# Performance work log

Measured on AMD Instinct MI355X. Metric: run time of the kernel, lower is better.

Reference implementation:

```python
import jax, jax.numpy as jnp
from jax import lax
import numpy as np

STRIDE = 1
PADDING = 1
DILATION = 1


def setup_inputs() -> dict:
    key = jax.random.key(0)
    k1, k2, k3, k4 = jax.random.split(key, 4)
    B, Cin, Cout, H, W, K, G = 32, 256, 256, 56, 56, 3, 8
    x = jax.random.normal(k1, (B, Cin, H, W), dtype=jnp.float32)
    conv = jax.random.normal(k2, (Cout, Cin, K, K), dtype=jnp.float32)
    S = jax.random.normal(k3, (Cin, G), dtype=jnp.float32)
    T = jax.random.normal(k4, (Cout, G), dtype=jnp.float32)
    return {"x": x, "conv": conv, "S": S, "T": T}


def reference(x, conv, S, T):
    # Faithful to FLGC.forward (training path).
    Cin = S.shape[0]
    Cout = T.shape[0]
    s_hat = jax.nn.softmax(S, axis=1)            # [Cin, G]
    t_hat = jax.nn.softmax(T, axis=1)            # [Cout, G]
    s = jnp.argmax(s_hat, axis=1)                # group id per input channel
    t = jnp.argmax(t_hat, axis=1)                # group id per output filter
    # Input channel c is scaled by s_hat[c, s[c]] inside its group.
    x_sc = x * s_hat[jnp.arange(Cin), s][None, :, None, None]
    # Filter o uses weight conv[o,c] * t_hat[o, t[o]] only where s[c] == t[o];
    # masking weights to zero elsewhere makes one dense conv equal the per-group convs.
    gate = (s[None, :] == t[:, None]).astype(conv.dtype)          # [Cout, Cin]
    w = conv * t_hat[jnp.arange(Cout), t][:, None, None, None] * gate[:, :, None, None]
    out_full = lax.conv_general_dilated(
        x_sc, w,
        window_strides=(STRIDE, STRIDE),
        padding=[(PADDING, PADDING), (PADDING, PADDING)],
        rhs_dilation=(DILATION, DILATION),
    )  # [B, Cout, H', W'], channel o = group-conv output of filter o
    # Original concatenates group outputs (channels ordered by perm = stable sort of t),
    # then indexes that with perm again: final[:, j] = out_full[:, perm[perm[j]]].
    perm = jnp.argsort(t * Cout + jnp.arange(Cout))  # stable group-major order
    return out_full[:, perm[perm]]
```

## Files before the change

kernel.cpp:

```cpp
#include <hip/hip_runtime.h>

#define M_SI    0
#define M_SO    256
#define M_CLIST 512
#define M_FLIST 768
#define M_DEST  1024
#define M_CBASE 1280
#define M_FBASE 1288
#define M_CCNT  1296
#define M_FCNT  1304
#define M_WOFFE 1312
#define WPACK_BYTE_OFF 16384
#define XR_BYTE_OFF   (4u << 20)
#define SLOT_ELEMS    3444736ull
#define SLOT_BYTES    (SLOT_ELEMS * 2ull)

typedef short bf16x8 __attribute__((ext_vector_type(8)));
typedef float f32x4  __attribute__((ext_vector_type(4)));

__device__ __forceinline__ unsigned short f2bf(float f) {
    unsigned u = __float_as_uint(f);
    u += 0x7fffu + ((u >> 16) & 1u);
    return (unsigned short)(u >> 16);
}

__device__ __forceinline__ void gl_lds16(const void* g, void* l) {
    __builtin_amdgcn_global_load_lds((const __attribute__((address_space(1))) unsigned int*)g,
                                     (__attribute__((address_space(3))) unsigned int*)l, 16, 0, 0);
}

__global__ __launch_bounds__(256) void flgc_setup(const float* __restrict__ S,
                                                  const float* __restrict__ T,
                                                  int* __restrict__ meta) {
    __shared__ float si[256], so[256];
    __shared__ int gin[256], gout[256];
    __shared__ int cnt_in[8], cnt_out[8], cb[8], fb[8];
    __shared__ int perm[256], destl[256];
    const int c = threadIdx.x;

    {
        float m = S[c * 8]; int am = 0;
        for (int k = 1; k < 8; ++k) { float v = S[c * 8 + k]; if (v > m) { m = v; am = k; } }
        float s = 0.f;
        for (int k = 0; k < 8; ++k) s += expf(S[c * 8 + k] - m);
        si[c] = 1.0f / s; gin[c] = am;
    }
    {
        float m = T[c * 8]; int am = 0;
        for (int k = 1; k < 8; ++k) { float v = T[c * 8 + k]; if (v > m) { m = v; am = k; } }
        float s = 0.f;
        for (int k = 0; k < 8; ++k) s += expf(T[c * 8 + k] - m);
        so[c] = 1.0f / s; gout[c] = am;
    }
    __syncthreads();
    const int g = gin[c], go = gout[c];
    int r1 = 0, r2 = 0;
    for (int i = 0; i < c; ++i) { r1 += (gin[i] == g); r2 += (gout[i] == go); }
    if (c < 8) {
        int n1 = 0, n2 = 0;
        for (int i = 0; i < 256; ++i) { n1 += (gin[i] == c); n2 += (gout[i] == c); }
        cnt_in[c] = n1; cnt_out[c] = n2;
    }
    __syncthreads();
    if (c == 0) {
        int a = 0, b = 0;
        for (int k = 0; k < 8; ++k) { cb[k] = a; a += cnt_in[k]; fb[k] = b; b += cnt_out[k]; }
    }
    __syncthreads();
    meta[M_CLIST + cb[g] + r1] = c;
    perm[fb[go] + r2] = c;
    __syncthreads();
    const int ppc = perm[perm[c]];
    destl[ppc] = c;
    __syncthreads();
    ((float*)meta)[M_SI + c] = si[c];
    ((float*)meta)[M_SO + c] = so[c];
    meta[M_FLIST + c] = perm[c];
    meta[M_DEST + c]  = destl[c];
    if (c < 8) {
        meta[M_CBASE + c] = cb[c];
        meta[M_FBASE + c] = fb[c];
        meta[M_CCNT + c]  = cnt_in[c];
        meta[M_FCNT + c]  = cnt_out[c];
    }
    if (c == 0) {
        int a = 0;
        for (int k = 0; k < 8; ++k) {
            meta[M_WOFFE + k] = a;
            const int nq  = (cnt_in[k] + 31) >> 5;
            const int mfa = (cnt_out[k] + 15) >> 4;
            a += nq * mfa * 9 * 512;
        }
        meta[M_WOFFE + 8] = a;
    }
}

__global__ void flgc_pack(const float* __restrict__ conv, const int* __restrict__ meta,
                          unsigned short* __restrict__ wpack) {
    const float* si = (const float*)meta + M_SI;
    const float* so = (const float*)meta + M_SO;
    const int total = meta[M_WOFFE + 8];
    for (int idx = blockIdx.x * blockDim.x + threadIdx.x; idx < total;
         idx += gridDim.x * blockDim.x) {
        int gg = 0;
        while (gg < 7 && idx >= meta[M_WOFFE + gg + 1]) ++gg;
        const int local = idx - meta[M_WOFFE + gg];
        const int fcnt = meta[M_FCNT + gg], ccnt = meta[M_CCNT + gg];
        const int mfall = (fcnt + 15) >> 4;
        const int fragidx = local >> 9, e = local & 511;
        const int lane = e >> 3, j = e & 7;
        const int tap = fragidx % 9, t2 = fragidx / 9;
        const int mf = t2 % mfall, q = t2 / mfall;
        const int fl = mf * 16 + (lane & 15);
        const int cl = q * 32 + (lane >> 4) * 8 + j;
        float v = 0.f;
        if (fl < fcnt && cl < ccnt) {
            const int F  = meta[M_FLIST + meta[M_FBASE + gg] + fl];
            const int CH = meta[M_CLIST + meta[M_CBASE + gg] + cl];
            v = conv[(F * 256 + CH) * 9 + tap] * si[CH] * so[F];
        }
        wpack[idx] = f2bf(v);
    }
}

__global__ __launch_bounds__(256) void flgc_reorder(const float* __restrict__ x,
                                                    const int* __restrict__ meta,
                                                    unsigned short* __restrict__ xr) {
    __shared__ float lds[32][65];
    const int r = blockIdx.x;
    const int b = blockIdx.y;
    const int slot = blockIdx.z;
    const int g = slot >> 1, q = slot & 1;
    const int ccnt = meta[M_CCNT + g];
    int nq = (ccnt + 31) >> 5; if (nq > 2) nq = 2;
    if (q >= nq) return;
    const int cbas = meta[M_CBASE + g];
    const int row = r - 1;
    const int colx = threadIdx.x & 63;
    const int cl0 = threadIdx.x >> 6;
    const int ic = colx - 1;
    const bool ok = ((unsigned)row < 56u) && ((unsigned)ic < 56u);

    int chn[8];
#pragma unroll
    for (int i = 0; i < 8; ++i) {
        const int cgl = q * 32 + cl0 + i * 4;
        chn[i] = (cgl < ccnt) ? meta[M_CLIST + cbas + cgl] : -1;
    }
    const float* xb = x + (size_t)b * 256 * 3136 + row * 56 + ic;
    float v[8];
#pragma unroll
    for (int i = 0; i < 8; ++i) v[i] = 0.f;
#pragma unroll
    for (int i = 0; i < 8; ++i)
        if (ok && chn[i] >= 0) v[i] = xb[(size_t)chn[i] * 3136];
#pragma unroll
    for (int i = 0; i < 8; ++i) lds[cl0 + i * 4][colx] = v[i];
    __syncthreads();

    unsigned short* dst = xr + (size_t)(slot * 32 + b) * 107648ull + r * 58 * 32;
    for (int i = threadIdx.x; i < 58 * 8; i += 256) {
        const int col = i >> 3, c8 = i & 7;
        const int chunk = c8 >> 1, lo = (c8 & 1) * 4;
        const int cl4 = chunk * 8 + lo;
        ushort4 pk = make_ushort4(f2bf(lds[cl4 + 0][col]), f2bf(lds[cl4 + 1][col]),
                                  f2bf(lds[cl4 + 2][col]), f2bf(lds[cl4 + 3][col]));
        const int schunk = chunk ^ ((col >> 1) & 3);
        *(ushort4*)&dst[col * 32 + schunk * 8 + lo] = pk;
    }
}


#define TAPS(Q)                                                                              \
    _Pragma("unroll") for (int tap = 0; tap < 9; ++tap) {                                    \
        const int dr = tap / 3, dc = tap - dr * 3;                                           \
        const int rowb = ((wv + dr) * 58) << 6;                                              \
        _Pragma("unroll") for (int cg = 0; cg < 4; ++cg) {                                   \
            const bf16x8 Bv = *(const bf16x8*)((const char*)xb + rowb + addrc[cg][dc]);      \
            _Pragma("unroll") for (int mf = 0; mf < MFE; ++mf)                               \
                acc[mf][cg] = __builtin_amdgcn_mfma_f32_16x16x32_bf16(                       \
                    A[Q][mf][tap], Bv, acc[mf][cg], 0, 0, 0);                                \
        }                                                                                    \
    }

template <int NQ, int MFE>
__device__ __forceinline__ void conv_pass(
    const unsigned short* __restrict__ wpack, const unsigned short* __restrict__ xr,
    float* __restrict__ out, unsigned short* xbufA, unsigned short* xbufB,
    const int (&ocv)[2][4], int b, int g, int z, int mf0, int mfall, int woffe,
    int lane, int wv) {
    const int nn = lane & 15, kg = lane >> 4;
    bf16x8 A[NQ][MFE][9];
#pragma unroll
    for (int q = 0; q < NQ; ++q)
#pragma unroll
        for (int mf = 0; mf < MFE; ++mf)
#pragma unroll
            for (int tap = 0; tap < 9; ++tap)
                A[q][mf][tap] = *(const bf16x8*)
                    &wpack[woffe + ((size_t)((q * mfall) + (mf0 + mf)) * 9 + tap) * 512 + lane * 8];
    int addrc[4][3];
#pragma unroll
    for (int cg = 0; cg < 4; ++cg)
#pragma unroll
        for (int dc = 0; dc < 3; ++dc) {
            int ccol = cg * 16 + nn + dc; if (ccol > 57) ccol = 57;
            addrc[cg][dc] = (ccol << 6) + ((kg ^ ((ccol >> 1) & 3)) << 4);
        }
    const int ns = (z < 2) ? 4 : 3;
    const int P = ns * NQ;
    const int base = wv * 348;
    {
        const char* src = (const char*)(xr + (size_t)((g * 2) * 32 + b) * 107648ull
                                        + (size_t)(4 * z) * 1856);
        char* dstb = (char*)xbufA;
#pragma unroll
        for (int j = 0; j < 5; ++j)
            gl_lds16(src + (size_t)(base + j * 64 + lane) * 16, dstb + (base + j * 64) * 16);
        if (lane < 28)
            gl_lds16(src + (size_t)(base + 320 + lane) * 16, dstb + (base + 320) * 16);
    }
    f32x4 acc[MFE][4];
    for (int p = 0; p < P; ++p) {
        if (p + 1 < P) {
            const int pn = p + 1;
            const int sp = z + 4 * (pn / NQ);
            const int qp = (NQ == 2) ? (pn & 1) : 0;
            const char* src = (const char*)(xr + (size_t)((g * 2 + qp) * 32 + b) * 107648ull
                                            + (size_t)(4 * sp) * 1856);
            char* dstb = (char*)((pn & 1) ? xbufB : xbufA);
#pragma unroll
            for (int j = 0; j < 5; ++j)
                gl_lds16(src + (size_t)(base + j * 64 + lane) * 16, dstb + (base + j * 64) * 16);
            if (lane < 28)
                gl_lds16(src + (size_t)(base + 320 + lane) * 16, dstb + (base + 320) * 16);
            asm volatile("s_waitcnt vmcnt(6)" ::: "memory");
        } else {
            asm volatile("s_waitcnt vmcnt(0)" ::: "memory");
        }
        __builtin_amdgcn_s_barrier();
        __builtin_amdgcn_sched_barrier(0);
        const unsigned short* xb = (p & 1) ? xbufB : xbufA;
        const int s = z + 4 * ((NQ == 2) ? (p >> 1) : p);
        if (NQ == 1 || (p & 1) == 0) {
#pragma unroll
            for (int mf = 0; mf < MFE; ++mf)
#pragma unroll
                for (int cg = 0; cg < 4; ++cg) acc[mf][cg] = (f32x4){0.f, 0.f, 0.f, 0.f};
        }
        if (NQ == 2 && (p & 1)) { TAPS(1) } else { TAPS(0) }
        if (NQ == 1 || (p & 1)) {
            const int h = 4 * s + wv;
#pragma unroll
            for (int mf = 0; mf < MFE; ++mf)
#pragma unroll
                for (int reg = 0; reg < 4; ++reg) {
                    const int oc = ocv[mf][reg];
                    if (oc >= 0) {
                        float* op = out + ((size_t)(b * 256 + oc) * 56 + h) * 56;
#pragma unroll
                        for (int cg = 0; cg < 4; ++cg) {
                            const int col = cg * 16 + nn;
                            if (col < 56) op[col] = acc[mf][cg][reg];
                        }
                    }
                }
        }
        __builtin_amdgcn_sched_barrier(0);
        __builtin_amdgcn_s_barrier();
    }
}

__global__ __launch_bounds__(256, 2) void flgc_conv_r(const int* __restrict__ meta,
                                                      const unsigned short* __restrict__ wpack,
                                                      const unsigned short* __restrict__ xr,
                                                      float* __restrict__ out) {
    __shared__ __align__(16) unsigned short xbufA[11136];
    __shared__ __align__(16) unsigned short xbufB[11136];
    const int b = blockIdx.x, g = blockIdx.y, z = blockIdx.z;
    const int tid = threadIdx.x, lane = tid & 63, wv = tid >> 6;
    const int ccnt = meta[M_CCNT + g], fcnt = meta[M_FCNT + g];
    const int fbas = meta[M_FBASE + g], woffe = meta[M_WOFFE + g];
    int nq = (ccnt + 31) >> 5; if (nq > 2) nq = 2;
    const int mfall = (fcnt + 15) >> 4;
    if (mfall == 0) return;
    const int nn = lane & 15;

    for (int mf0 = 0; mf0 < mfall; mf0 += 2) {
        const int mfe = min(2, mfall - mf0);
        int ocv[2][4];
#pragma unroll
        for (int mf = 0; mf < 2; ++mf)
#pragma unroll
            for (int reg = 0; reg < 4; ++reg) {
                const int fl = (mf0 + mf) * 16 + (lane >> 4) * 4 + reg;
                ocv[mf][reg] = (mf < mfe && fl < fcnt)
                    ? meta[M_DEST + meta[M_FLIST + fbas + fl]] : -1;
            }
        if (nq == 0) {
            const int ns = (z < 2) ? 4 : 3;
            for (int si = 0; si < ns; ++si) {
                const int h = 4 * (z + 4 * si) + wv;
#pragma unroll
                for (int mf = 0; mf < 2; ++mf)
#pragma unroll
                    for (int reg = 0; reg < 4; ++reg)
                        if (ocv[mf][reg] >= 0) {
                            float* op = out + ((size_t)(b * 256 + ocv[mf][reg]) * 56 + h) * 56;
#pragma unroll
                            for (int cg = 0; cg < 4; ++cg) {
                                const int col = cg * 16 + nn;
                                if (col < 56) op[col] = 0.f;
                            }
                        }
            }
            continue;
        }
        if (nq == 1) {
            if (mfe == 2) conv_pass<1, 2>(wpack, xr, out, xbufA, xbufB, ocv, b, g, z, mf0, mfall, woffe, lane, wv);
            else          conv_pass<1, 1>(wpack, xr, out, xbufA, xbufB, ocv, b, g, z, mf0, mfall, woffe, lane, wv);
        } else {
            if (mfe == 2) conv_pass<2, 2>(wpack, xr, out, xbufA, xbufB, ocv, b, g, z, mf0, mfall, woffe, lane, wv);
            else          conv_pass<2, 1>(wpack, xr, out, xbufA, xbufB, ocv, b, g, z, mf0, mfall, woffe, lane, wv);
        }
    }
}

__global__ __launch_bounds__(256, 2) void flgc_conv_mfma(const float* __restrict__ x,
                                                         const int* __restrict__ meta,
                                                         const unsigned short* __restrict__ wpack,
                                                         float* __restrict__ out) {
    __shared__ __align__(16) unsigned short xlds[10 * 4 * 64 * 8];
    __shared__ __align__(16) unsigned short wlds[4 * 9 * 512];
    const int g = blockIdx.z, b = blockIdx.y, h0 = blockIdx.x * 8;
    const int tid = threadIdx.x, lane = tid & 63, wv = tid >> 6;
    const int ccnt = meta[M_CCNT + g], fcnt = meta[M_FCNT + g];
    const int cbas = meta[M_CBASE + g], fbas = meta[M_FBASE + g];
    const int woffe = meta[M_WOFFE + g];
    const int nq = (ccnt + 31) >> 5, mfall = (fcnt + 15) >> 4;
    if (mfall == 0) return;
    const int n = lane & 15, kgl = lane >> 4;
    const int prow = 2 * wv + (n >> 3);
    const int pcol = n & 7;

    for (int mf0 = 0; mf0 < mfall; mf0 += 4) {
        const int mfe = min(4, mfall - mf0);
        f32x4 acc[4][7];
#pragma unroll
        for (int mf = 0; mf < 4; ++mf)
#pragma unroll
            for (int cg = 0; cg < 7; ++cg) acc[mf][cg] = (f32x4){0.f, 0.f, 0.f, 0.f};

        for (int q = 0; q < nq; ++q) {
            __syncthreads();
            for (int widx = wv; widx < mfe * 9; widx += 4) {
                const int mf = widx / 9, tap = widx - mf * 9;
                const unsigned short* src =
                    wpack + woffe + (((q * mfall) + mf0 + mf) * 9 + tap) * 512 + lane * 8;
                *(bf16x8*)&wlds[(mf * 9 + tap) * 512 + lane * 8] = *(const bf16x8*)src;
            }
            for (int i = tid; i < 80 * 64; i += 256) {
                const int colx = i & 63, t = i >> 6;
                const int rr = t >> 3, cq = t & 7;
                const int c0 = q * 32 + cq * 4;
                const int row = h0 + rr - 1, ic = colx - 1;
                float v0 = 0.f, v1 = 0.f, v2 = 0.f, v3 = 0.f;
                if ((unsigned)row < 56u && (unsigned)ic < 56u) {
                    const float* xp = x + (size_t)(b * 256) * 3136 + row * 56 + ic;
                    if (c0 + 0 < ccnt) v0 = xp[(size_t)meta[M_CLIST + cbas + c0 + 0] * 3136];
                    if (c0 + 1 < ccnt) v1 = xp[(size_t)meta[M_CLIST + cbas + c0 + 1] * 3136];
                    if (c0 + 2 < ccnt) v2 = xp[(size_t)meta[M_CLIST + cbas + c0 + 2] * 3136];
                    if (c0 + 3 < ccnt) v3 = xp[(size_t)meta[M_CLIST + cbas + c0 + 3] * 3136];
                }
                ushort4 pk = make_ushort4(f2bf(v0), f2bf(v1), f2bf(v2), f2bf(v3));
                *(ushort4*)&xlds[(((rr * 4 + (cq >> 1)) * 64 + colx) << 3) + ((cq & 1) << 2)] = pk;
            }
            __syncthreads();
#pragma unroll
            for (int tap = 0; tap < 9; ++tap) {
                const int dr = tap / 3, dcp = tap - dr * 3;
                bf16x8 A[4];
#pragma unroll
                for (int mf = 0; mf < 4; ++mf)
                    if (mf < mfe)
                        A[mf] = *(bf16x8*)&wlds[(mf * 9 + tap) * 512 + lane * 8];
                const int row_r = prow + dr;
                const int xbase = ((row_r * 4 + kgl) * 64) << 3;
#pragma unroll
                for (int cg = 0; cg < 7; ++cg) {
                    const int cc = cg * 8 + pcol + dcp;
                    const bf16x8 B = *(bf16x8*)&xlds[xbase + (cc << 3)];
#pragma unroll
                    for (int mf = 0; mf < 4; ++mf)
                        if (mf < mfe)
                            acc[mf][cg] = __builtin_amdgcn_mfma_f32_16x16x32_bf16(
                                A[mf], B, acc[mf][cg], 0, 0, 0);
                }
            }
        }
#pragma unroll
        for (int mf = 0; mf < 4; ++mf) {
            if (mf < mfe) {
#pragma unroll
                for (int reg = 0; reg < 4; ++reg) {
                    const int fl = (mf0 + mf) * 16 + (lane >> 4) * 4 + reg;
                    if (fl < fcnt) {
                        const int F  = meta[M_FLIST + fbas + fl];
                        const int oc = meta[M_DEST + F];
                        float* op = out + ((size_t)(b * 256 + oc) * 56 + (h0 + prow)) * 56 + pcol;
#pragma unroll
                        for (int cg = 0; cg < 7; ++cg)
                            op[cg * 8] = acc[mf][cg][reg];
                    }
                }
            }
        }
    }
}

extern "C" void kernel_launch(void* const* d_in, const int* in_sizes, int n_in,
                              void* d_out, int out_size, void* d_ws, size_t ws_size,
                              hipStream_t stream) {
    const float* x    = (const float*)d_in[0];
    const float* conv = (const float*)d_in[1];
    const float* S    = (const float*)d_in[2];
    const float* T    = (const float*)d_in[3];
    float* out = (float*)d_out;
    int* meta = (int*)d_ws;
    unsigned short* wpack = (unsigned short*)((char*)d_ws + WPACK_BYTE_OFF);
    unsigned short* xr    = (unsigned short*)((char*)d_ws + XR_BYTE_OFF);

    flgc_setup<<<1, 256, 0, stream>>>(S, T, meta);
    flgc_pack<<<256, 256, 0, stream>>>(conv, meta, wpack);

    const size_t need = (size_t)XR_BYTE_OFF + 16ull * SLOT_BYTES + 65536;
    if (ws_size >= need) {
        flgc_reorder<<<dim3(58, 32, 16), 256, 0, stream>>>(x, meta, xr);
        flgc_conv_r<<<dim3(32, 8, 4), 256, 0, stream>>>(meta, wpack, xr, out);
    } else {
        flgc_conv_mfma<<<dim3(7, 32, 8), 256, 0, stream>>>(x, meta, wpack, out);
    }
}
```

Baseline: 127.2 us.

## Reload weight fragments per pass and widen filter tile to three MFMA blocks

Weight fragments are now loaded from global memory on every pipeline step instead of being held in registers for the whole pass. The register space this frees lets each block process up to three 16-filter MFMA tiles at once instead of two, so the input row tile staged in LDS is reused across more filters and fewer passes over the input are needed. The channel-chunk count becomes a runtime value instead of a template parameter. The cost is repeated global or cache loads of the weights on each step, plus possible register pressure from the larger accumulator array.

```diff
diff --git a/kernel.cpp b/kernel.cpp
--- a/kernel.cpp
+++ b/kernel.cpp
@@ -170,35 +170,13 @@
     }
 }
 
-
-#define TAPS(Q)                                                                              \
-    _Pragma("unroll") for (int tap = 0; tap < 9; ++tap) {                                    \
-        const int dr = tap / 3, dc = tap - dr * 3;                                           \
-        const int rowb = ((wv + dr) * 58) << 6;                                              \
-        _Pragma("unroll") for (int cg = 0; cg < 4; ++cg) {                                   \
-            const bf16x8 Bv = *(const bf16x8*)((const char*)xb + rowb + addrc[cg][dc]);      \
-            _Pragma("unroll") for (int mf = 0; mf < MFE; ++mf)                               \
-                acc[mf][cg] = __builtin_amdgcn_mfma_f32_16x16x32_bf16(                       \
-                    A[Q][mf][tap], Bv, acc[mf][cg], 0, 0, 0);                                \
-        }                                                                                    \
-    }
-
-template <int NQ, int MFE>
+template <int MFE>
 __device__ __forceinline__ void conv_pass(
     const unsigned short* __restrict__ wpack, const unsigned short* __restrict__ xr,
     float* __restrict__ out, unsigned short* xbufA, unsigned short* xbufB,
-    const int (&ocv)[2][4], int b, int g, int z, int mf0, int mfall, int woffe,
+    const int (&ocv)[3][4], int b, int g, int z, int nq, int mf0, int mfall, int woffe,
     int lane, int wv) {
     const int nn = lane & 15, kg = lane >> 4;
-    bf16x8 A[NQ][MFE][9];
-#pragma unroll
-    for (int q = 0; q < NQ; ++q)
-#pragma unroll
-        for (int mf = 0; mf < MFE; ++mf)
-#pragma unroll
-            for (int tap = 0; tap < 9; ++tap)
-                A[q][mf][tap] = *(const bf16x8*)
-                    &wpack[woffe + ((size_t)((q * mfall) + (mf0 + mf)) * 9 + tap) * 512 + lane * 8];
     int addrc[4][3];
 #pragma unroll
     for (int cg = 0; cg < 4; ++cg)
@@ -208,7 +186,7 @@
             addrc[cg][dc] = (ccol << 6) + ((kg ^ ((ccol >> 1) & 3)) << 4);
         }
     const int ns = (z < 2) ? 4 : 3;
-    const int P = ns * NQ;
+    const int P = ns * nq;
     const int base = wv * 348;
     {
         const char* src = (const char*)(xr + (size_t)((g * 2) * 32 + b) * 107648ull
@@ -222,10 +200,23 @@
     }
     f32x4 acc[MFE][4];
     for (int p = 0; p < P; ++p) {
+        const int q = (nq == 2) ? (p & 1) : 0;
+        const int s = z + 4 * ((nq == 2) ? (p >> 1) : p);
+        bf16x8 A[MFE][9];
+        {
+            const unsigned short* ap =
+                wpack + woffe + ((size_t)(q * mfall + mf0) * 9) * 512 + lane * 8;
+#pragma unroll
+            for (int mf = 0; mf < MFE; ++mf)
+#pragma unroll
+                for (int tap = 0; tap < 9; ++tap)
+                    A[mf][tap] = *(const bf16x8*)(ap + (size_t)(mf * 9 + tap) * 512);
+        }
+        __builtin_amdgcn_sched_barrier(0);
         if (p + 1 < P) {
             const int pn = p + 1;
-            const int sp = z + 4 * (pn / NQ);
-            const int qp = (NQ == 2) ? (pn & 1) : 0;
+            const int qp = (nq == 2) ? (pn & 1) : 0;
+            const int sp = z + 4 * ((nq == 2) ? (pn >> 1) : pn);
             const char* src = (const char*)(xr + (size_t)((g * 2 + qp) * 32 + b) * 107648ull
                                             + (size_t)(4 * sp) * 1856);
             char* dstb = (char*)((pn & 1) ? xbufB : xbufA);
@@ -241,15 +232,26 @@
         __builtin_amdgcn_s_barrier();
         __builtin_amdgcn_sched_barrier(0);
         const unsigned short* xb = (p & 1) ? xbufB : xbufA;
-        const int s = z + 4 * ((NQ == 2) ? (p >> 1) : p);
-        if (NQ == 1 || (p & 1) == 0) {
+        if (q == 0) {
 #pragma unroll
             for (int mf = 0; mf < MFE; ++mf)
 #pragma unroll
                 for (int cg = 0; cg < 4; ++cg) acc[mf][cg] = (f32x4){0.f, 0.f, 0.f, 0.f};
         }
-        if (NQ == 2 && (p & 1)) { TAPS(1) } else { TAPS(0) }
-        if (NQ == 1 || (p & 1)) {
+#pragma unroll
+        for (int tap = 0; tap < 9; ++tap) {
+            const int dr = tap / 3, dc = tap - dr * 3;
+            const int rowb = ((wv + dr) * 58) << 6;
+#pragma unroll
+            for (int cg = 0; cg < 4; ++cg) {
+                const bf16x8 Bv = *(const bf16x8*)((const char*)xb + rowb + addrc[cg][dc]);
+#pragma unroll
+                for (int mf = 0; mf < MFE; ++mf)
+                    acc[mf][cg] = __builtin_amdgcn_mfma_f32_16x16x32_bf16(
+                        A[mf][tap], Bv, acc[mf][cg], 0, 0, 0);
+            }
+        }
+        if (q == nq - 1) {
             const int h = 4 * s + wv;
 #pragma unroll
             for (int mf = 0; mf < MFE; ++mf)
@@ -286,11 +288,11 @@
     if (mfall == 0) return;
     const int nn = lane & 15;
 
-    for (int mf0 = 0; mf0 < mfall; mf0 += 2) {
-        const int mfe = min(2, mfall - mf0);
-        int ocv[2][4];
-#pragma unroll
-        for (int mf = 0; mf < 2; ++mf)
+    for (int mf0 = 0; mf0 < mfall; mf0 += 3) {
+        const int mfe = min(3, mfall - mf0);
+        int ocv[3][4];
+#pragma unroll
+        for (int mf = 0; mf < 3; ++mf)
 #pragma unroll
             for (int reg = 0; reg < 4; ++reg) {
                 const int fl = (mf0 + mf) * 16 + (lane >> 4) * 4 + reg;
@@ -302,7 +304,7 @@
             for (int si = 0; si < ns; ++si) {
                 const int h = 4 * (z + 4 * si) + wv;
 #pragma unroll
-                for (int mf = 0; mf < 2; ++mf)
+                for (int mf = 0; mf < 3; ++mf)
 #pragma unroll
                     for (int reg = 0; reg < 4; ++reg)
                         if (ocv[mf][reg] >= 0) {
@@ -316,13 +318,9 @@
             }
             continue;
         }
-        if (nq == 1) {
-            if (mfe == 2) conv_pass<1, 2>(wpack, xr, out, xbufA, xbufB, ocv, b, g, z, mf0, mfall, woffe, lane, wv);
-            else          conv_pass<1, 1>(wpack, xr, out, xbufA, xbufB, ocv, b, g, z, mf0, mfall, woffe, lane, wv);
-        } else {
-            if (mfe == 2) conv_pass<2, 2>(wpack, xr, out, xbufA, xbufB, ocv, b, g, z, mf0, mfall, woffe, lane, wv);
-            else          conv_pass<2, 1>(wpack, xr, out, xbufA, xbufB, ocv, b, g, z, mf0, mfall, woffe, lane, wv);
-        }
+        if (mfe == 3)      conv_pass<3>(wpack, xr, out, xbufA, xbufB, ocv, b, g, z, nq, mf0, mfall, woffe, lane, wv);
+        else if (mfe == 2) conv_pass<2>(wpack, xr, out, xbufA, xbufB, ocv, b, g, z, nq, mf0, mfall, woffe, lane, wv);
+        else               conv_pass<1>(wpack, xr, out, xbufA, xbufB, ocv, b, g, z, nq, mf0, mfall, woffe, lane, wv);
     }
 }
 
```

Measured after the change: 107.0 us. 15.9% less time.
